# Kernel optimization log

Hardware: AMD Instinct MI355X
Metric: run time of the kernel (lower is better)

## Reference

```python
import jax, jax.numpy as jnp
import numpy as np

DIM = 256
HEADS = 8
CAMS = 6
MINSIZE = 25  # AdaptiveAvgPool2d output size = min(feature_map_size)


def layernorm(x, g, b, eps=1e-5):
    mu = x.mean(-1, keepdims=True)
    var = ((x - mu) ** 2).mean(-1, keepdims=True)
    return (x - mu) / jnp.sqrt(var + eps) * g + b


def setup_inputs() -> dict:
    key = jax.random.key(0)
    ks = jax.random.split(key, 16)
    d, n = DIM, CAMS
    s = 0.02
    inp = {}
    inp["q"] = jax.random.normal(ks[0], (2, n, d, 50, 50), jnp.float32)
    inp["k"] = jax.random.normal(ks[1], (2, n, d, 50, 50), jnp.float32)
    inp["v"] = jax.random.normal(ks[2], (2, n, d, 50, 50), jnp.float32)
    inp["Wq"] = jax.random.normal(ks[3], (d, d), jnp.float32) * s
    inp["bq"] = jnp.zeros((d,), jnp.float32)
    inp["Wk"] = jax.random.normal(ks[4], (d, d), jnp.float32) * s
    inp["bk"] = jnp.zeros((d,), jnp.float32)
    inp["Wv"] = jax.random.normal(ks[5], (d, d), jnp.float32) * s
    inp["bv"] = jnp.zeros((d,), jnp.float32)
    inp["Wproj"] = jax.random.normal(ks[6], (n * d, d), jnp.float32) * s
    inp["bproj"] = jnp.zeros((d,), jnp.float32)
    inp["Waddq"] = jax.random.normal(ks[7], (n * d, d), jnp.float32) * s
    inp["baddq"] = jnp.zeros((d,), jnp.float32)
    inp["W1"] = jax.random.normal(ks[8], (d, 2 * d), jnp.float32) * s
    inp["b1"] = jnp.zeros((2 * d,), jnp.float32)
    inp["W2"] = jax.random.normal(ks[9], (2 * d, d), jnp.float32) * s
    inp["b2"] = jnp.zeros((d,), jnp.float32)
    inp["g_pre"] = jnp.ones((n * d,), jnp.float32)
    inp["b_pre"] = jnp.zeros((n * d,), jnp.float32)
    inp["g_norm"] = jnp.ones((d,), jnp.float32)
    inp["b_norm"] = jnp.zeros((d,), jnp.float32)
    return inp


def reference(q, k, v, Wq, bq, Wk, bk, Wv, bv, Wproj, bproj, Waddq, baddq,
              W1, b1, W2, b2, g_pre, b_pre, g_norm, b_norm):
    B, n, d, H, W = q.shape
    m = HEADS
    dh = d // m
    Q = H * W

    # residual query path: (b n d H W) -> (b HW (n d)) -> add_qproj -> (b HW d)
    add_q = jnp.transpose(q, (0, 3, 4, 1, 2)).reshape(B, Q, n * d) @ Waddq + baddq

    # queries: (b n d H W) -> (b n HW d) -> to_q
    qf = jnp.transpose(q, (0, 1, 3, 4, 2)).reshape(B, n, Q, d) @ Wq + bq

    # adaptive avg pool to MINSIZE (exact 2x2 bins since 50 = 2*25)
    def pool(t):
        _, _, _, h, w = t.shape
        return t.reshape(B, n, d, MINSIZE, h // MINSIZE, MINSIZE, w // MINSIZE).mean((4, 6))

    kp = pool(k)  # (b n d 25 25)
    vp = pool(v)
    K = MINSIZE * MINSIZE
    # (avg pool commutes with the pointwise linear to_k/to_v)
    kf = jnp.transpose(kp, (0, 1, 3, 4, 2)).reshape(B, n, K, d) @ Wk + bk
    vf = jnp.transpose(vp, (0, 1, 3, 4, 2)).reshape(B, n, K, d) @ Wv + bv

    # split heads
    qh = qf.reshape(B, n, Q, m, dh)
    kh = kf.reshape(B, n, K, m, dh)
    vh = vf.reshape(B, n, K, m, dh)

    # per-camera scores, softmax jointly over concatenated camera keys
    scores = (dh ** -0.5) * jnp.einsum('bnqmd,bnkmd->bmqnk', qh, kh)  # (B,m,Q,n,K)
    attn = jax.nn.softmax(scores.reshape(B, m, Q, n * K), axis=-1).reshape(B, m, Q, n, K)

    # per-camera attention output, concat cams (and heads within each cam) -> (B,Q,n*d)
    out = jnp.einsum('bmqnk,bnkmd->bqnmd', attn, vh).reshape(B, Q, n * d)

    x = layernorm(out, g_pre, b_pre) @ Wproj + bproj  # (B,Q,d)
    x = x + add_q
    h1 = jax.nn.gelu(x @ W1 + b1, approximate=False)
    x = x + layernorm(h1 @ W2 + b2, g_norm, b_norm)
    return jnp.transpose(x.reshape(B, H, W, d), (0, 3, 1, 2))  # (B,d,H,W)
```

## Files before the change

### kernel.cpp

```cpp
#include <hip/hip_runtime.h>
#include <math.h>

#define BATCH 2
#define NCAM 6
#define DIM 256
#define HEADS 8
#define DH 32
#define HW 2500
#define KP 625
#define NDIM (NCAM*DIM)

#define SCALE_LOG2E 0.25503488494404f

typedef __attribute__((ext_vector_type(8))) short short8;
typedef __attribute__((ext_vector_type(4))) float f32x4;

__device__ __forceinline__ short f2bf(float f) {
    union { float f; unsigned u; } v; v.f = f;
    unsigned r = v.u + 0x7fffu + ((v.u >> 16) & 1u);
    return (short)(r >> 16);
}
__device__ __forceinline__ float bf2f(short h) {
    union { unsigned u; float f; } v; v.u = ((unsigned)(unsigned short)h) << 16;
    return v.f;
}
__device__ __forceinline__ float exp2_hw(float x) {
    return __builtin_amdgcn_exp2f(x);
}

struct WJ { const float* src; short* dst; int K, N; };
struct WArgs { WJ j[7]; };

__global__ __launch_bounds__(256) void prep_all(
    const float* __restrict__ q, const float* __restrict__ k,
    const float* __restrict__ v, short* __restrict__ qbf,
    short* __restrict__ kpbf, short* __restrict__ vpbf, WArgs wa)
{
    __shared__ float t[32][33];
    const int tx = threadIdx.x & 31, ty = threadIdx.x >> 5;
    int i = blockIdx.x;
    if (i < 7584) {
        int slab = i / 632, rem = i % 632;
        int hwB = (rem % 79) * 32, dB = (rem / 79) * 32;
        const float* src = q + (size_t)slab * 640000;
#pragma unroll
        for (int ii = 0; ii < 32; ii += 8) {
            int hw = hwB + tx;
            t[ty + ii][tx] = (hw < HW) ? src[(size_t)(dB + ty + ii) * HW + hw] : 0.f;
        }
        __syncthreads();
#pragma unroll
        for (int ii = 0; ii < 32; ii += 8) {
            int hw = hwB + ty + ii;
            if (hw < HW)
                qbf[((size_t)slab * HW + hw) * DIM + dB + tx] = f2bf(t[tx][ty + ii]);
        }
    } else if (i < 11424) {
        int i2 = i - 7584;
        const float* base; short* dst;
        if (i2 < 1920) { base = k; dst = kpbf; }
        else           { base = v; dst = vpbf; i2 -= 1920; }
        int slab = i2 / 160, rem = i2 % 160;
        int kpB = (rem % 20) * 32, dB = (rem / 20) * 32;
        const float* src = base + (size_t)slab * 640000;
        dst += (size_t)slab * (KP * DIM);
#pragma unroll
        for (int ii = 0; ii < 32; ii += 8) {
            int kp = kpB + tx;
            float val = 0.f;
            if (kp < KP) {
                int r2 = (kp / 25) * 2, c2 = (kp % 25) * 2;
                const float* p0 = src + (size_t)(dB + ty + ii) * HW + r2 * 50 + c2;
                val = 0.25f * (p0[0] + p0[1] + p0[50] + p0[51]);
            }
            t[ty + ii][tx] = val;
        }
        __syncthreads();
#pragma unroll
        for (int ii = 0; ii < 32; ii += 8) {
            int kp = kpB + ty + ii;
            if (kp < KP)
                dst[(size_t)kp * DIM + dB + tx] = f2bf(t[tx][ty + ii]);
        }
    } else {
        int wi = i - 11424;
        WJ jb = wa.j[0];
        for (int jj = 0; jj < 7; jj++) {
            jb = wa.j[jj];
            int cnt = (jb.K >> 5) * (jb.N >> 5);
            if (wi < cnt) break;
            wi -= cnt;
        }
        int tn = jb.N >> 5;
        int nB = (wi % tn) * 32, kB = (wi / tn) * 32;
#pragma unroll
        for (int ii = 0; ii < 32; ii += 8)
            t[ty + ii][tx] = jb.src[(size_t)(kB + ty + ii) * jb.N + nB + tx];
        __syncthreads();
#pragma unroll
        for (int ii = 0; ii < 32; ii += 8)
            jb.dst[(size_t)(nB + ty + ii) * jb.K + kB + tx] = f2bf(t[tx][ty + ii]);
    }
}

struct GJob { const short* A; const short* Bt; const float* bias;
              short* Cb; float* Cf; int M, K, yb, mode; float smul; };
struct GArgs { GJob j[4]; };

__global__ __launch_bounds__(256) void gemm_in(GArgs ga) {
    GJob jb = ga.j[blockIdx.z];
    if ((int)blockIdx.y >= jb.yb) return;
    __shared__ short As[128 * 32];
    __shared__ short Bs[64 * 32];

    const int tid  = threadIdx.x;
    const int nB   = blockIdx.x * 64;
    const int rB   = blockIdx.y * 128;
    const int w    = tid >> 6;
    const int lane = tid & 63;
    const int l15  = lane & 15;
    const int quad = lane >> 4;
    const int M = jb.M, K = jb.K;

    f32x4 acc[2][4];
#pragma unroll
    for (int i = 0; i < 2; i++)
#pragma unroll
        for (int jt = 0; jt < 4; jt++) acc[i][jt] = (f32x4){0.f, 0.f, 0.f, 0.f};

    const int ra = tid >> 1, k0 = (tid & 1) * 16;
    const int rga = rB + ra;
    const int bb = rga / 2500, hwp = rga % 2500;
    const int nb_ = tid >> 2, gkb = tid & 3;

    short8 pa0 = {0,0,0,0,0,0,0,0}, pa1 = pa0, pb = pa0;
    if (rga < M) {
        if (jb.mode) {
            int cam = k0 >> 8, c = k0 & 255;
            const short* p = &jb.A[(((size_t)(bb * 6 + cam)) * HW + hwp) * DIM + c];
            pa0 = *(const short8*)p; pa1 = *(const short8*)(p + 8);
        } else {
            const short* p = &jb.A[(size_t)rga * K + k0];
            pa0 = *(const short8*)p; pa1 = *(const short8*)(p + 8);
        }
    }
    pb = *(const short8*)&jb.Bt[(size_t)(nB + nb_) * K + gkb * 8];

    for (int kB = 0; kB < K; kB += 32) {
        __syncthreads();
        {
            int g0 = k0 >> 3;
            *(short8*)&As[ra * 32 + ((g0 ^ (ra & 3)) << 3)]       = pa0;
            *(short8*)&As[ra * 32 + (((g0 + 1) ^ (ra & 3)) << 3)] = pa1;
            *(short8*)&Bs[nb_ * 32 + ((gkb ^ (nb_ & 3)) << 3)]    = pb;
        }
        __syncthreads();
        int kN = kB + 32;
        if (kN < K) {
            if (rga < M) {
                if (jb.mode) {
                    int kk = kN + k0;
                    int cam = kk >> 8, c = kk & 255;
                    const short* p = &jb.A[(((size_t)(bb * 6 + cam)) * HW + hwp) * DIM + c];
                    pa0 = *(const short8*)p; pa1 = *(const short8*)(p + 8);
                } else {
                    const short* p = &jb.A[(size_t)rga * K + kN + k0];
                    pa0 = *(const short8*)p; pa1 = *(const short8*)(p + 8);
                }
            }
            pb = *(const short8*)&jb.Bt[(size_t)(nB + nb_) * K + kN + gkb * 8];
        }
        short8 af[2], bfr[4];
#pragma unroll
        for (int i = 0; i < 2; i++) {
            int m = w * 32 + i * 16 + l15;
            af[i] = *(const short8*)&As[m * 32 + ((quad ^ (m & 3)) << 3)];
        }
#pragma unroll
        for (int jt = 0; jt < 4; jt++) {
            int n = jt * 16 + l15;
            bfr[jt] = *(const short8*)&Bs[n * 32 + ((quad ^ (n & 3)) << 3)];
        }
#pragma unroll
        for (int i = 0; i < 2; i++)
#pragma unroll
            for (int jt = 0; jt < 4; jt++)
                acc[i][jt] = __builtin_amdgcn_mfma_f32_16x16x32_bf16(
                    af[i], bfr[jt], acc[i][jt], 0, 0, 0);
    }
#pragma unroll
    for (int i = 0; i < 2; i++) {
        int rbase = rB + w * 32 + i * 16 + quad * 4;
#pragma unroll
        for (int jt = 0; jt < 4; jt++) {
            int col = nB + jt * 16 + l15;
            float bcol = jb.bias[col];
#pragma unroll
            for (int reg = 0; reg < 4; reg++) {
                int rr = rbase + reg;
                if (rr < M) {
                    float vv = (acc[i][jt][reg] + bcol) * jb.smul;
                    if (jb.Cb) jb.Cb[(size_t)rr * 256 + col] = f2bf(vv);
                    else       jb.Cf[(size_t)rr * 256 + col] = vv;
                }
            }
        }
    }
}

template<int EPI, int WF32, int WBF>
__global__ __launch_bounds__(256) void mgemm_bf(
    const short* __restrict__ A, const short* __restrict__ Bt,
    const float* __restrict__ bias, const float* __restrict__ res,
    float* __restrict__ C, short* __restrict__ C2, int M, int N, int K)
{
    __shared__ short As[128 * 32];
    __shared__ short Bs[64 * 32];

    const int tid  = threadIdx.x;
    const int nB   = blockIdx.x * 64;
    const int rB   = blockIdx.y * 128;
    const int w    = tid >> 6;
    const int lane = tid & 63;
    const int l15  = lane & 15;
    const int quad = lane >> 4;

    f32x4 acc[2][4];
#pragma unroll
    for (int i = 0; i < 2; i++)
#pragma unroll
        for (int jt = 0; jt < 4; jt++) acc[i][jt] = (f32x4){0.f, 0.f, 0.f, 0.f};

    const int ra = tid >> 1, k0 = (tid & 1) * 16;
    const int rga = rB + ra;
    const int nb_ = tid >> 2, gkb = tid & 3;

    short8 pa0 = {0,0,0,0,0,0,0,0}, pa1 = pa0, pb = pa0;
    if (rga < M) {
        const short* p = &A[(size_t)rga * K + k0];
        pa0 = *(const short8*)p; pa1 = *(const short8*)(p + 8);
    }
    pb = *(const short8*)&Bt[(size_t)(nB + nb_) * K + gkb * 8];

    for (int kB = 0; kB < K; kB += 32) {
        __syncthreads();
        {
            int g0 = k0 >> 3;
            *(short8*)&As[ra * 32 + ((g0 ^ (ra & 3)) << 3)]       = pa0;
            *(short8*)&As[ra * 32 + (((g0 + 1) ^ (ra & 3)) << 3)] = pa1;
            *(short8*)&Bs[nb_ * 32 + ((gkb ^ (nb_ & 3)) << 3)]    = pb;
        }
        __syncthreads();
        int kN = kB + 32;
        if (kN < K) {
            if (rga < M) {
                const short* p = &A[(size_t)rga * K + kN + k0];
                pa0 = *(const short8*)p; pa1 = *(const short8*)(p + 8);
            }
            pb = *(const short8*)&Bt[(size_t)(nB + nb_) * K + kN + gkb * 8];
        }
        short8 af[2], bfr[4];
#pragma unroll
        for (int i = 0; i < 2; i++) {
            int m = w * 32 + i * 16 + l15;
            af[i] = *(const short8*)&As[m * 32 + ((quad ^ (m & 3)) << 3)];
        }
#pragma unroll
        for (int jt = 0; jt < 4; jt++) {
            int n = jt * 16 + l15;
            bfr[jt] = *(const short8*)&Bs[n * 32 + ((quad ^ (n & 3)) << 3)];
        }
#pragma unroll
        for (int i = 0; i < 2; i++)
#pragma unroll
            for (int jt = 0; jt < 4; jt++)
                acc[i][jt] = __builtin_amdgcn_mfma_f32_16x16x32_bf16(
                    af[i], bfr[jt], acc[i][jt], 0, 0, 0);
    }
#pragma unroll
    for (int i = 0; i < 2; i++) {
        int rbase = rB + w * 32 + i * 16 + quad * 4;
#pragma unroll
        for (int jt = 0; jt < 4; jt++) {
            int col = nB + jt * 16 + l15;
            float bcol = bias[col];
#pragma unroll
            for (int reg = 0; reg < 4; reg++) {
                int rr = rbase + reg;
                if (rr < M) {
                    float vv = acc[i][jt][reg] + bcol;
                    if (EPI == 1) vv = 0.5f * vv * (1.f + erff(vv * 0.70710678118654752f));
                    if (EPI == 2) vv += res[(size_t)rr * N + col];
                    if (WF32) C[(size_t)rr * N + col] = vv;
                    if (WBF)  C2[(size_t)rr * N + col] = f2bf(vv);
                }
            }
        }
    }
}

#define TQA 64
#define CH 64
#define VSTR 72

__global__ __launch_bounds__(256) void attn_mfma(
    const short* __restrict__ qf, const short* __restrict__ kf,
    const short* __restrict__ vf, short* __restrict__ attn_out,
    float* __restrict__ Zp)
{
    const int qt  = blockIdx.x;
    const int bm  = blockIdx.y;
    const int cam = blockIdx.z;
    const int b = bm >> 3, m = bm & 7;
    const int q0 = qt * TQA;
    const int tid = threadIdx.x;
    const int w = tid >> 6, lane = tid & 63;
    const int l15 = lane & 15, quad = lane >> 4;

    __shared__ __align__(16) short Ks[CH][DH];
    __shared__ __align__(16) short Vt[DH][VSTR];

    const size_t slab = (size_t)(b * 6 + cam);

    int qrow = q0 + w * 16 + l15;
    int qcl  = qrow < HW ? qrow : HW - 1;
    const short8 aq = *(const short8*)&qf[(slab * HW + qcl) * DIM + m * DH + quad * 8];

    const short* kb = kf + slab * KP * DIM + m * DH;
    const short* vb = vf + slab * KP * DIM + m * DH;

    f32x4 oacc[2];
    oacc[0] = (f32x4){0.f, 0.f, 0.f, 0.f};
    oacc[1] = (f32x4){0.f, 0.f, 0.f, 0.f};
    float zp = 0.f;

    const int kl = tid >> 2, d8 = (tid & 3) * 8;
    const int jtw  = ((kl >> 5) & 1) | (((kl >> 2) & 1) << 1);
    const int rw   = (((kl >> 3) & 3) << 2) | (kl & 3);
    const int krow = jtw * 16 + rw;
    const int kp2 = tid >> 3, dv = (tid & 7) * 4;
    const int vcol2 = (((kp2 >> 2) ^ (dv >> 3)) << 3) | ((2 * kp2) & 7);

    for (int c0 = 0; c0 < KP; c0 += CH) {
        __syncthreads();
        {
            int key = c0 + kl;
            short8 kv8 = {0, 0, 0, 0, 0, 0, 0, 0};
            if (key < KP) kv8 = *(const short8*)&kb[(size_t)key * DIM + d8];
            *(short8*)&Ks[krow][d8] = kv8;

            int k0v = c0 + 2 * kp2;
            uint2 a0 = {0u, 0u}, a1 = {0u, 0u};
            if (k0v < KP)     a0 = *(const uint2*)&vb[(size_t)k0v * DIM + dv];
            if (k0v + 1 < KP) a1 = *(const uint2*)&vb[(size_t)(k0v + 1) * DIM + dv];
            *(unsigned*)&Vt[dv + 0][vcol2] = __builtin_amdgcn_perm(a1.x, a0.x, 0x05040100u);
            *(unsigned*)&Vt[dv + 1][vcol2] = __builtin_amdgcn_perm(a1.x, a0.x, 0x07060302u);
            *(unsigned*)&Vt[dv + 2][vcol2] = __builtin_amdgcn_perm(a1.y, a0.y, 0x05040100u);
            *(unsigned*)&Vt[dv + 3][vcol2] = __builtin_amdgcn_perm(a1.y, a0.y, 0x07060302u);
        }
        __syncthreads();
        f32x4 sfragT[4];
#pragma unroll
        for (int jt = 0; jt < 4; jt++) {
            short8 bk8 = *(const short8*)&Ks[jt * 16 + l15][quad * 8];
            sfragT[jt] = __builtin_amdgcn_mfma_f32_16x16x32_bf16(
                bk8, aq, (f32x4){0.f, 0.f, 0.f, 0.f}, 0, 0, 0);
        }
        union PA { unsigned u[4]; short8 s8; } pa[2];
        if (c0 + CH <= KP) {
#pragma unroll
            for (int jt = 0; jt < 4; jt++) {
                float e0 = exp2_hw(sfragT[jt][0]);
                float e1 = exp2_hw(sfragT[jt][1]);
                float e2 = exp2_hw(sfragT[jt][2]);
                float e3 = exp2_hw(sfragT[jt][3]);
                zp += (e0 + e1) + (e2 + e3);
                asm("v_cvt_pk_bf16_f32 %0, %1, %2"
                    : "=v"(pa[jt & 1].u[(jt >> 1) * 2]) : "v"(e0), "v"(e1));
                asm("v_cvt_pk_bf16_f32 %0, %1, %2"
                    : "=v"(pa[jt & 1].u[(jt >> 1) * 2 + 1]) : "v"(e2), "v"(e3));
            }
        } else {
            int kq8 = c0 + quad * 8;
#pragma unroll
            for (int jt = 0; jt < 4; jt++) {
                int kb0 = kq8 + (jt & 1) * 32 + ((jt >> 1) << 2);
                float e0 = (kb0 + 0 < KP) ? exp2_hw(sfragT[jt][0]) : 0.f;
                float e1 = (kb0 + 1 < KP) ? exp2_hw(sfragT[jt][1]) : 0.f;
                float e2 = (kb0 + 2 < KP) ? exp2_hw(sfragT[jt][2]) : 0.f;
                float e3 = (kb0 + 3 < KP) ? exp2_hw(sfragT[jt][3]) : 0.f;
                zp += (e0 + e1) + (e2 + e3);
                asm("v_cvt_pk_bf16_f32 %0, %1, %2"
                    : "=v"(pa[jt & 1].u[(jt >> 1) * 2]) : "v"(e0), "v"(e1));
                asm("v_cvt_pk_bf16_f32 %0, %1, %2"
                    : "=v"(pa[jt & 1].u[(jt >> 1) * 2 + 1]) : "v"(e2), "v"(e3));
            }
        }
#pragma unroll
        for (int ks = 0; ks < 2; ks++) {
#pragma unroll
            for (int nt = 0; nt < 2; nt++) {
                int dhn = nt * 16 + l15;
                int pgrp = ((ks * 4 + quad) ^ (dhn >> 3));
                short8 bv8 = *(const short8*)&Vt[dhn][pgrp << 3];
                oacc[nt] = __builtin_amdgcn_mfma_f32_16x16x32_bf16(
                    pa[ks].s8, bv8, oacc[nt], 0, 0, 0);
            }
        }
    }
    zp += __shfl_xor(zp, 16, 64);
    zp += __shfl_xor(zp, 32, 64);
    if (quad == 0) {
        int q = q0 + w * 16 + l15;
        if (q < HW) Zp[((size_t)bm * 6 + cam) * HW + q] = zp;
    }
#pragma unroll
    for (int reg = 0; reg < 4; reg++) {
        int q = q0 + w * 16 + quad * 4 + reg;
        if (q < HW) {
            size_t rowb = ((size_t)b * HW + q) * NDIM + cam * DIM + m * DH;
            attn_out[rowb + l15]      = f2bf(oacc[0][reg]);
            attn_out[rowb + 16 + l15] = f2bf(oacc[1][reg]);
        }
    }
}

__global__ __launch_bounds__(256) void ln_pre_kernel(
    const short* __restrict__ xin, short* __restrict__ lnbf,
    const float* __restrict__ Zp,
    const float* __restrict__ g, const float* __restrict__ bt)
{
    const int row = blockIdx.x;
    const int tid = threadIdx.x;
    const int b = row / 2500, q = row % 2500;
    __shared__ float zinv[8];
    if (tid < 8) {
        float z = 0.f;
#pragma unroll
        for (int cam = 0; cam < 6; cam++)
            z += Zp[((size_t)(b * 8 + tid) * 6 + cam) * HW + q];
        zinv[tid] = 1.f / z;
    }
    __syncthreads();
    const short* p = xin + (size_t)row * NDIM;
    float v[6];
    float s = 0.f, ss = 0.f;
#pragma unroll
    for (int i = 0; i < 6; i++) {
        int c = tid + i * 256;
        v[i] = bf2f(p[c]) * zinv[(c >> 5) & 7];
        s += v[i]; ss += v[i] * v[i];
    }
    __shared__ float rs[4], rss[4];
    int lane = tid & 63, wid = tid >> 6;
#pragma unroll
    for (int o = 32; o > 0; o >>= 1) { s += __shfl_down(s, o); ss += __shfl_down(ss, o); }
    if (lane == 0) { rs[wid] = s; rss[wid] = ss; }
    __syncthreads();
    s = rs[0] + rs[1] + rs[2] + rs[3];
    ss = rss[0] + rss[1] + rss[2] + rss[3];
    float mu = s * (1.f / NDIM);
    float var = ss * (1.f / NDIM) - mu * mu;
    float inv = rsqrtf(var + 1e-5f);
#pragma unroll
    for (int i = 0; i < 6; i++) {
        int c = tid + i * 256;
        lnbf[(size_t)row * NDIM + c] = f2bf((v[i] - mu) * inv * g[c] + bt[c]);
    }
}

__global__ __launch_bounds__(256) void final_kernel2(
    const float* __restrict__ x, const float* __restrict__ y2,
    const float* __restrict__ g, const float* __restrict__ bt,
    float* __restrict__ out)
{
    __shared__ float T[256][33];
    __shared__ float ps[32][8], pss[32][8];
    __shared__ float mu_s[32], inv_s[32];
    const int tid = threadIdx.x;
    const int rl = tid & 31, seg = tid >> 5;
    const int r0 = blockIdx.x * 32;
    const int row = r0 + rl;
    const bool ok = row < 5000;

    float4 yv[8];
    float s = 0.f, ss = 0.f;
    if (ok) {
        const float4* yp = (const float4*)(y2 + (size_t)row * DIM + seg * 32);
#pragma unroll
        for (int j = 0; j < 8; j++) {
            yv[j] = yp[j];
            s += yv[j].x + yv[j].y + yv[j].z + yv[j].w;
            ss += yv[j].x * yv[j].x + yv[j].y * yv[j].y
                + yv[j].z * yv[j].z + yv[j].w * yv[j].w;
        }
    } else {
#pragma unroll
        for (int j = 0; j < 8; j++) yv[j] = (float4){0, 0, 0, 0};
    }
    ps[rl][seg] = s; pss[rl][seg] = ss;
    __syncthreads();
    if (tid < 32) {
        float a = 0.f, b2 = 0.f;
#pragma unroll
        for (int j = 0; j < 8; j++) { a += ps[tid][j]; b2 += pss[tid][j]; }
        float mu = a * (1.f / DIM);
        float var = b2 * (1.f / DIM) - mu * mu;
        mu_s[tid] = mu;
        inv_s[tid] = rsqrtf(var + 1e-5f);
    }
    __syncthreads();
    if (ok) {
        float mu = mu_s[rl], inv = inv_s[rl];
        const float4* xp = (const float4*)(x + (size_t)row * DIM + seg * 32);
#pragma unroll
        for (int j = 0; j < 8; j++) {
            float4 xv = xp[j];
            int c = seg * 32 + j * 4;
            T[c + 0][rl] = xv.x + (yv[j].x - mu) * inv * g[c + 0] + bt[c + 0];
            T[c + 1][rl] = xv.y + (yv[j].y - mu) * inv * g[c + 1] + bt[c + 1];
            T[c + 2][rl] = xv.z + (yv[j].z - mu) * inv * g[c + 2] + bt[c + 2];
            T[c + 3][rl] = xv.w + (yv[j].w - mu) * inv * g[c + 3] + bt[c + 3];
        }
    }
    __syncthreads();
    const int w = tid >> 6, lane = tid & 63;
    const int hl = lane & 31, ch = lane >> 5;
    const int rr = r0 + hl;
    if (rr < 5000) {
        int b = rr / 2500, hw = rr % 2500;
        size_t obase = (size_t)b * 640000 + hw;
#pragma unroll
        for (int it = 0; it < 32; it++) {
            int c = it * 8 + w * 2 + ch;
            out[obase + (size_t)c * 2500] = T[c][hl];
        }
    }
}

extern "C" void kernel_launch(void* const* d_in, const int* in_sizes, int n_in,
                              void* d_out, int out_size, void* d_ws, size_t ws_size,
                              hipStream_t stream)
{
    const float* q     = (const float*)d_in[0];
    const float* k     = (const float*)d_in[1];
    const float* v     = (const float*)d_in[2];
    const float* Wq    = (const float*)d_in[3];
    const float* bq    = (const float*)d_in[4];
    const float* Wk    = (const float*)d_in[5];
    const float* bk    = (const float*)d_in[6];
    const float* Wv    = (const float*)d_in[7];
    const float* bv    = (const float*)d_in[8];
    const float* Wproj = (const float*)d_in[9];
    const float* bproj = (const float*)d_in[10];
    const float* Waddq = (const float*)d_in[11];
    const float* baddq = (const float*)d_in[12];
    const float* W1    = (const float*)d_in[13];
    const float* b1    = (const float*)d_in[14];
    const float* W2    = (const float*)d_in[15];
    const float* b2    = (const float*)d_in[16];
    const float* g_pre = (const float*)d_in[17];
    const float* b_pre = (const float*)d_in[18];
    const float* g_nrm = (const float*)d_in[19];
    const float* b_nrm = (const float*)d_in[20];
    float* out = (float*)d_out;

    float* ws = (float*)d_ws;
    short* qf_a   = (short*)(ws);
    short* lnbf   = (short*)(ws);
    short* qbf    = (short*)(ws + 3840000);
    short* kf_a   = (short*)(ws + 7680000);
    short* kpbf   = (short*)(ws + 8640000);
    short* vf_a   = (short*)(ws + 9600000);
    short* vpbf   = (short*)(ws + 10560000);
    float* add_q  = ws + 11520000;
    short* attn_o = (short*)(ws + 12800000);
    short* xbf    = (short*)(ws + 12800000);
    short* h1bf   = (short*)(ws + 13440000);
    float* x      = ws + 20480000;
    float* Zp     = ws + 21760000;
    short* eW     = (short*)(ws + 22000000);
    short* Wq_t    = eW;
    short* Wk_t    = eW + 65536;
    short* Wv_t    = eW + 131072;
    short* Waddq_t = eW + 196608;
    short* lW     = (short*)(ws + 22295000);
    short* Wproj_t = lW;
    short* W1_t    = lW + 393216;
    short* W2_t    = lW + 524288;
    float* y2     = ws + 22625000;

    dim3 blk(256);

    {
        WArgs wa;
        wa.j[0] = {Wq,    Wq_t,    256,  256};
        wa.j[1] = {Wk,    Wk_t,    256,  256};
        wa.j[2] = {Wv,    Wv_t,    256,  256};
        wa.j[3] = {Waddq, Waddq_t, 1536, 256};
        wa.j[4] = {Wproj, Wproj_t, 1536, 256};
        wa.j[5] = {W1,    W1_t,    256,  512};
        wa.j[6] = {W2,    W2_t,    512,  256};
        prep_all<<<dim3(12640), blk, 0, stream>>>(q, k, v, qbf, kpbf, vpbf, wa);
    }
    {
        GArgs ga;
        ga.j[0] = {qbf,  Wq_t,    bq,    qf_a, nullptr, 30000, 256,  235, 0, SCALE_LOG2E};
        ga.j[1] = {kpbf, Wk_t,    bk,    kf_a, nullptr, 7500,  256,  59,  0, 1.0f};
        ga.j[2] = {vpbf, Wv_t,    bv,    vf_a, nullptr, 7500,  256,  59,  0, 1.0f};
        ga.j[3] = {qbf,  Waddq_t, baddq, nullptr, add_q, 5000, 1536, 40,  1, 1.0f};
        gemm_in<<<dim3(4, 235, 4), blk, 0, stream>>>(ga);
    }
    attn_mfma<<<dim3(40, 16, 6), blk, 0, stream>>>(qf_a, kf_a, vf_a, attn_o, Zp);
    ln_pre_kernel<<<dim3(5000), blk, 0, stream>>>(attn_o, lnbf, Zp, g_pre, b_pre);
    mgemm_bf<2, 1, 1><<<dim3(4, 40), blk, 0, stream>>>(
        lnbf, Wproj_t, bproj, add_q, x, xbf, 5000, 256, 1536);
    mgemm_bf<1, 0, 1><<<dim3(8, 40), blk, 0, stream>>>(
        xbf, W1_t, b1, nullptr, nullptr, h1bf, 5000, 512, 256);
    mgemm_bf<0, 1, 0><<<dim3(4, 40), blk, 0, stream>>>(
        h1bf, W2_t, b2, nullptr, y2, nullptr, 5000, 256, 512);
    final_kernel2<<<dim3(157), blk, 0, stream>>>(x, y2, g_nrm, b_nrm, out);
}
```

Measured before the change: 323.0 us.

## Split add_q GEMM along K, flatten gemm_in grid with XCD-aware block remap

The add_q GEMM (K=1536) is split into two K-halves that write separate fp32 partial outputs. The second partial is summed into the Wproj GEMM epilogue as an extra residual. gemm_in now uses a flat 1D grid with prefix-sum job lookup, replacing the old 3D grid where many blocks exited early. Long-K jobs are placed first, and block IDs are remapped so consecutive tiles land on the same XCD. The aim is better load balance and fewer idle blocks, at the cost of an extra fp32 partial buffer and one more residual read.

```diff
diff --git a/kernel.cpp b/kernel.cpp
--- a/kernel.cpp
+++ b/kernel.cpp
@@ -104,12 +104,129 @@
 }
 
 struct GJob { const short* A; const short* Bt; const float* bias;
-              short* Cb; float* Cf; int M, K, yb, mode; float smul; };
-struct GArgs { GJob j[4]; };
+              short* Cb; float* Cf; int M, Ks, Kl, kOff, mode; float smul; };
+struct GArgs { GJob j[5]; int base[6]; };
 
 __global__ __launch_bounds__(256) void gemm_in(GArgs ga) {
-    GJob jb = ga.j[blockIdx.z];
-    if ((int)blockIdx.y >= jb.yb) return;
+    int bid;
+    {
+        const int nwg = ga.base[5];
+        int orig = blockIdx.x;
+        int q8 = nwg >> 3, r8 = nwg & 7;
+        int xcd = orig & 7, idx = orig >> 3;
+        bid = (xcd < r8 ? xcd * (q8 + 1) : r8 * (q8 + 1) + (xcd - r8) * q8) + idx;
+    }
+    int jj = 0;
+    while (bid >= ga.base[jj + 1]) jj++;
+    GJob jb = ga.j[jj];
+    const int local = bid - ga.base[jj];
+
+    __shared__ short As[128 * 32];
+    __shared__ short Bs[64 * 32];
+
+    const int tid  = threadIdx.x;
+    const int nB   = (local & 3) * 64;
+    const int rB   = (local >> 2) * 128;
+    const int w    = tid >> 6;
+    const int lane = tid & 63;
+    const int l15  = lane & 15;
+    const int quad = lane >> 4;
+    const int M = jb.M, Ks = jb.Ks, Kl = jb.Kl, kOff = jb.kOff;
+
+    f32x4 acc[2][4];
+#pragma unroll
+    for (int i = 0; i < 2; i++)
+#pragma unroll
+        for (int jt = 0; jt < 4; jt++) acc[i][jt] = (f32x4){0.f, 0.f, 0.f, 0.f};
+
+    const int ra = tid >> 1, k0 = (tid & 1) * 16;
+    const int rga = rB + ra;
+    const int bb = rga / 2500, hwp = rga % 2500;
+    const int nb_ = tid >> 2, gkb = tid & 3;
+
+    short8 pa0 = {0,0,0,0,0,0,0,0}, pa1 = pa0, pb = pa0;
+    if (rga < M) {
+        if (jb.mode) {
+            int kk = kOff + k0;
+            int cam = kk >> 8, c = kk & 255;
+            const short* p = &jb.A[(((size_t)(bb * 6 + cam)) * HW + hwp) * DIM + c];
+            pa0 = *(const short8*)p; pa1 = *(const short8*)(p + 8);
+        } else {
+            const short* p = &jb.A[(size_t)rga * Ks + kOff + k0];
+            pa0 = *(const short8*)p; pa1 = *(const short8*)(p + 8);
+        }
+    }
+    pb = *(const short8*)&jb.Bt[(size_t)(nB + nb_) * Ks + kOff + gkb * 8];
+
+    for (int kB = 0; kB < Kl; kB += 32) {
+        __syncthreads();
+        {
+            int g0 = k0 >> 3;
+            *(short8*)&As[ra * 32 + ((g0 ^ (ra & 3)) << 3)]       = pa0;
+            *(short8*)&As[ra * 32 + (((g0 + 1) ^ (ra & 3)) << 3)] = pa1;
+            *(short8*)&Bs[nb_ * 32 + ((gkb ^ (nb_ & 3)) << 3)]    = pb;
+        }
+        __syncthreads();
+        int kN = kB + 32;
+        if (kN < Kl) {
+            if (rga < M) {
+                if (jb.mode) {
+                    int kk = kOff + kN + k0;
+                    int cam = kk >> 8, c = kk & 255;
+                    const short* p = &jb.A[(((size_t)(bb * 6 + cam)) * HW + hwp) * DIM + c];
+                    pa0 = *(const short8*)p; pa1 = *(const short8*)(p + 8);
+                } else {
+                    const short* p = &jb.A[(size_t)rga * Ks + kOff + kN + k0];
+                    pa0 = *(const short8*)p; pa1 = *(const short8*)(p + 8);
+                }
+            }
+            pb = *(const short8*)&jb.Bt[(size_t)(nB + nb_) * Ks + kOff + kN + gkb * 8];
+        }
+        short8 af[2], bfr[4];
+#pragma unroll
+        for (int i = 0; i < 2; i++) {
+            int m = w * 32 + i * 16 + l15;
+            af[i] = *(const short8*)&As[m * 32 + ((quad ^ (m & 3)) << 3)];
+        }
+#pragma unroll
+        for (int jt = 0; jt < 4; jt++) {
+            int n = jt * 16 + l15;
+            bfr[jt] = *(const short8*)&Bs[n * 32 + ((quad ^ (n & 3)) << 3)];
+        }
+#pragma unroll
+        for (int i = 0; i < 2; i++)
+#pragma unroll
+            for (int jt = 0; jt < 4; jt++)
+                acc[i][jt] = __builtin_amdgcn_mfma_f32_16x16x32_bf16(
+                    af[i], bfr[jt], acc[i][jt], 0, 0, 0);
+    }
+#pragma unroll
+    for (int i = 0; i < 2; i++) {
+        int rbase = rB + w * 32 + i * 16 + quad * 4;
+#pragma unroll
+        for (int jt = 0; jt < 4; jt++) {
+            int col = nB + jt * 16 + l15;
+            float bcol = jb.bias ? jb.bias[col] : 0.f;
+#pragma unroll
+            for (int reg = 0; reg < 4; reg++) {
+                int rr = rbase + reg;
+                if (rr < M) {
+                    float vv = (acc[i][jt][reg] + bcol) * jb.smul;
+                    if (jb.Cb) jb.Cb[(size_t)rr * 256 + col] = f2bf(vv);
+                    else       jb.Cf[(size_t)rr * 256 + col] = vv;
+                }
+            }
+        }
+    }
+}
+
+template<int EPI, int WF32, int WBF>
+__global__ __launch_bounds__(256) void mgemm_bf(
+    const short* __restrict__ A, const short* __restrict__ Bt,
+    const float* __restrict__ bias, const float* __restrict__ res,
+    const float* __restrict__ res2,
+    float* __restrict__ C, short* __restrict__ C2, int M, int N, int K)
+{
     __shared__ short As[128 * 32];
     __shared__ short Bs[64 * 32];
 
@@ -120,7 +237,6 @@
     const int lane = tid & 63;
     const int l15  = lane & 15;
     const int quad = lane >> 4;
-    const int M = jb.M, K = jb.K;
 
     f32x4 acc[2][4];
 #pragma unroll
@@ -130,21 +246,14 @@
 
     const int ra = tid >> 1, k0 = (tid & 1) * 16;
     const int rga = rB + ra;
-    const int bb = rga / 2500, hwp = rga % 2500;
     const int nb_ = tid >> 2, gkb = tid & 3;
 
     short8 pa0 = {0,0,0,0,0,0,0,0}, pa1 = pa0, pb = pa0;
     if (rga < M) {
-        if (jb.mode) {
-            int cam = k0 >> 8, c = k0 & 255;
-            const short* p = &jb.A[(((size_t)(bb * 6 + cam)) * HW + hwp) * DIM + c];
-            pa0 = *(const short8*)p; pa1 = *(const short8*)(p + 8);
-        } else {
-            const short* p = &jb.A[(size_t)rga * K + k0];
-            pa0 = *(const short8*)p; pa1 = *(const short8*)(p + 8);
-        }
-    }
-    pb = *(const short8*)&jb.Bt[(size_t)(nB + nb_) * K + gkb * 8];
+        const short* p = &A[(size_t)rga * K + k0];
+        pa0 = *(const short8*)p; pa1 = *(const short8*)(p + 8);
+    }
+    pb = *(const short8*)&Bt[(size_t)(nB + nb_) * K + gkb * 8];
 
     for (int kB = 0; kB < K; kB += 32) {
         __syncthreads();
@@ -158,102 +267,6 @@
         int kN = kB + 32;
         if (kN < K) {
             if (rga < M) {
-                if (jb.mode) {
-                    int kk = kN + k0;
-                    int cam = kk >> 8, c = kk & 255;
-                    const short* p = &jb.A[(((size_t)(bb * 6 + cam)) * HW + hwp) * DIM + c];
-                    pa0 = *(const short8*)p; pa1 = *(const short8*)(p + 8);
-                } else {
-                    const short* p = &jb.A[(size_t)rga * K + kN + k0];
-                    pa0 = *(const short8*)p; pa1 = *(const short8*)(p + 8);
-                }
-            }
-            pb = *(const short8*)&jb.Bt[(size_t)(nB + nb_) * K + kN + gkb * 8];
-        }
-        short8 af[2], bfr[4];
-#pragma unroll
-        for (int i = 0; i < 2; i++) {
-            int m = w * 32 + i * 16 + l15;
-            af[i] = *(const short8*)&As[m * 32 + ((quad ^ (m & 3)) << 3)];
-        }
-#pragma unroll
-        for (int jt = 0; jt < 4; jt++) {
-            int n = jt * 16 + l15;
-            bfr[jt] = *(const short8*)&Bs[n * 32 + ((quad ^ (n & 3)) << 3)];
-        }
-#pragma unroll
-        for (int i = 0; i < 2; i++)
-#pragma unroll
-            for (int jt = 0; jt < 4; jt++)
-                acc[i][jt] = __builtin_amdgcn_mfma_f32_16x16x32_bf16(
-                    af[i], bfr[jt], acc[i][jt], 0, 0, 0);
-    }
-#pragma unroll
-    for (int i = 0; i < 2; i++) {
-        int rbase = rB + w * 32 + i * 16 + quad * 4;
-#pragma unroll
-        for (int jt = 0; jt < 4; jt++) {
-            int col = nB + jt * 16 + l15;
-            float bcol = jb.bias[col];
-#pragma unroll
-            for (int reg = 0; reg < 4; reg++) {
-                int rr = rbase + reg;
-                if (rr < M) {
-                    float vv = (acc[i][jt][reg] + bcol) * jb.smul;
-                    if (jb.Cb) jb.Cb[(size_t)rr * 256 + col] = f2bf(vv);
-                    else       jb.Cf[(size_t)rr * 256 + col] = vv;
-                }
-            }
-        }
-    }
-}
-
-template<int EPI, int WF32, int WBF>
-__global__ __launch_bounds__(256) void mgemm_bf(
-    const short* __restrict__ A, const short* __restrict__ Bt,
-    const float* __restrict__ bias, const float* __restrict__ res,
-    float* __restrict__ C, short* __restrict__ C2, int M, int N, int K)
-{
-    __shared__ short As[128 * 32];
-    __shared__ short Bs[64 * 32];
-
-    const int tid  = threadIdx.x;
-    const int nB   = blockIdx.x * 64;
-    const int rB   = blockIdx.y * 128;
-    const int w    = tid >> 6;
-    const int lane = tid & 63;
-    const int l15  = lane & 15;
-    const int quad = lane >> 4;
-
-    f32x4 acc[2][4];
-#pragma unroll
-    for (int i = 0; i < 2; i++)
-#pragma unroll
-        for (int jt = 0; jt < 4; jt++) acc[i][jt] = (f32x4){0.f, 0.f, 0.f, 0.f};
-
-    const int ra = tid >> 1, k0 = (tid & 1) * 16;
-    const int rga = rB + ra;
-    const int nb_ = tid >> 2, gkb = tid & 3;
-
-    short8 pa0 = {0,0,0,0,0,0,0,0}, pa1 = pa0, pb = pa0;
-    if (rga < M) {
-        const short* p = &A[(size_t)rga * K + k0];
-        pa0 = *(const short8*)p; pa1 = *(const short8*)(p + 8);
-    }
-    pb = *(const short8*)&Bt[(size_t)(nB + nb_) * K + gkb * 8];
-
-    for (int kB = 0; kB < K; kB += 32) {
-        __syncthreads();
-        {
-            int g0 = k0 >> 3;
-            *(short8*)&As[ra * 32 + ((g0 ^ (ra & 3)) << 3)]       = pa0;
-            *(short8*)&As[ra * 32 + (((g0 + 1) ^ (ra & 3)) << 3)] = pa1;
-            *(short8*)&Bs[nb_ * 32 + ((gkb ^ (nb_ & 3)) << 3)]    = pb;
-        }
-        __syncthreads();
-        int kN = kB + 32;
-        if (kN < K) {
-            if (rga < M) {
                 const short* p = &A[(size_t)rga * K + kN + k0];
                 pa0 = *(const short8*)p; pa1 = *(const short8*)(p + 8);
             }
@@ -290,7 +303,10 @@
                 if (rr < M) {
                     float vv = acc[i][jt][reg] + bcol;
                     if (EPI == 1) vv = 0.5f * vv * (1.f + erff(vv * 0.70710678118654752f));
-                    if (EPI == 2) vv += res[(size_t)rr * N + col];
+                    if (EPI == 2) {
+                        vv += res[(size_t)rr * N + col];
+                        if (res2) vv += res2[(size_t)rr * N + col];
+                    }
                     if (WF32) C[(size_t)rr * N + col] = vv;
                     if (WBF)  C2[(size_t)rr * N + col] = f2bf(vv);
                 }
@@ -577,6 +593,7 @@
     short* attn_o = (short*)(ws + 12800000);
     short* xbf    = (short*)(ws + 12800000);
     short* h1bf   = (short*)(ws + 13440000);
+    float* add_q2 = ws + 16640000;
     float* x      = ws + 20480000;
     float* Zp     = ws + 21760000;
     short* eW     = (short*)(ws + 22000000);
@@ -605,19 +622,23 @@
     }
     {
         GArgs ga;
-        ga.j[0] = {qbf,  Wq_t,    bq,    qf_a, nullptr, 30000, 256,  235, 0, SCALE_LOG2E};
-        ga.j[1] = {kpbf, Wk_t,    bk,    kf_a, nullptr, 7500,  256,  59,  0, 1.0f};
-        ga.j[2] = {vpbf, Wv_t,    bv,    vf_a, nullptr, 7500,  256,  59,  0, 1.0f};
-        ga.j[3] = {qbf,  Waddq_t, baddq, nullptr, add_q, 5000, 1536, 40,  1, 1.0f};
-        gemm_in<<<dim3(4, 235, 4), blk, 0, stream>>>(ga);
+        ga.j[0] = {qbf,  Waddq_t, baddq,   nullptr, add_q,  5000,  1536, 768, 0,   1, 1.0f};
+        ga.j[1] = {qbf,  Waddq_t, nullptr, nullptr, add_q2, 5000,  1536, 768, 768, 1, 1.0f};
+        ga.j[2] = {qbf,  Wq_t,    bq,      qf_a,    nullptr, 30000, 256, 256, 0,   0, SCALE_LOG2E};
+        ga.j[3] = {kpbf, Wk_t,    bk,      kf_a,    nullptr, 7500,  256, 256, 0,   0, 1.0f};
+        ga.j[4] = {vpbf, Wv_t,    bv,      vf_a,    nullptr, 7500,  256, 256, 0,   0, 1.0f};
+        int cnt[5] = {160, 160, 940, 236, 236};
+        ga.base[0] = 0;
+        for (int i = 0; i < 5; i++) ga.base[i + 1] = ga.base[i] + cnt[i];
+        gemm_in<<<dim3(ga.base[5]), blk, 0, stream>>>(ga);
     }
     attn_mfma<<<dim3(40, 16, 6), blk, 0, stream>>>(qf_a, kf_a, vf_a, attn_o, Zp);
     ln_pre_kernel<<<dim3(5000), blk, 0, stream>>>(attn_o, lnbf, Zp, g_pre, b_pre);
     mgemm_bf<2, 1, 1><<<dim3(4, 40), blk, 0, stream>>>(
-        lnbf, Wproj_t, bproj, add_q, x, xbf, 5000, 256, 1536);
+        lnbf, Wproj_t, bproj, add_q, add_q2, x, xbf, 5000, 256, 1536);
     mgemm_bf<1, 0, 1><<<dim3(8, 40), blk, 0, stream>>>(
-        xbf, W1_t, b1, nullptr, nullptr, h1bf, 5000, 512, 256);
+        xbf, W1_t, b1, nullptr, nullptr, nullptr, h1bf, 5000, 512, 256);
     mgemm_bf<0, 1, 0><<<dim3(4, 40), blk, 0, stream>>>(
-        h1bf, W2_t, b2, nullptr, y2, nullptr, 5000, 256, 512);
+        h1bf, W2_t, b2, nullptr, nullptr, y2, nullptr, 5000, 256, 512);
     final_kernel2<<<dim3(157), blk, 0, stream>>>(x, y2, g_nrm, b_nrm, out);
 }
```

Result: slower. 334.1 us (+3.4%).
